# Kernel optimization log

Measured on AMD Instinct MI355X. Metric: run time of the kernel, lower is better.

Reference implementation:

```python
import jax, jax.numpy as jnp
import numpy as np

HEADS = 4
HID = 610
KER = 50  # cov2KerSize
NEG_SLOPE = 0.2


def gat_layer(x, src, dst, w, b, att_src, att_dst, n_nodes):
    # x: [N, Fin], w: [HEADS*HID, Fin], att_*: [1, HEADS, HID], b: [HID]
    h = (x @ w.T).reshape(n_nodes, HEADS, HID)               # [N,H,D]
    a_src = (h * att_src).sum(-1)                            # [N,H]
    a_dst = (h * att_dst).sum(-1)                            # [N,H]
    alpha = jax.nn.leaky_relu(a_src[src] + a_dst[dst], NEG_SLOPE)  # [E,H]
    # softmax over edges grouped by destination node
    m = jax.ops.segment_max(alpha, dst, num_segments=n_nodes)
    e = jnp.exp(alpha - m[dst])
    denom = jax.ops.segment_sum(e, dst, num_segments=n_nodes)
    a = e / (denom[dst] + 1e-16)                             # [E,H]
    msg = h[src] * a[:, :, None]                             # [E,H,D]
    out = jax.ops.segment_sum(msg, dst, num_segments=n_nodes)  # [N,H,D]
    return out.mean(axis=1) + b                              # [N,D] (concat=False)


def setup_inputs() -> dict:
    key = jax.random.key(0)
    ks = jax.random.split(key, 16)
    N, E, FIN, NOUT = 20000, 100000, 128, 86
    x = jax.random.normal(ks[0], (N, FIN), dtype=jnp.float32)
    edge_index = jax.random.randint(ks[1], (2, E), 0, N, dtype=jnp.int64)
    def kaiming(k, shape, fan_in):
        return jax.random.normal(k, shape, dtype=jnp.float32) * np.float32(np.sqrt(2.0 / fan_in))
    w0 = kaiming(ks[2], (HEADS * HID, FIN), FIN)
    b0 = jnp.zeros((HID,), jnp.float32)
    att_src0 = kaiming(ks[3], (1, HEADS, HID), HID)
    att_dst0 = kaiming(ks[4], (1, HEADS, HID), HID)
    w2 = kaiming(ks[5], (HEADS * HID, HID), HID)
    b2 = jnp.zeros((HID,), jnp.float32)
    att_src1 = kaiming(ks[6], (1, HEADS, HID), HID)
    att_dst1 = kaiming(ks[7], (1, HEADS, HID), HID)
    w4 = kaiming(ks[8], (1, 1, 2, KER), 2 * KER)
    b4 = jnp.zeros((1,), jnp.float32)
    w6 = kaiming(ks[9], (1, 1, KER), KER)
    b6 = jnp.zeros((1,), jnp.float32)
    w8 = kaiming(ks[10], (NOUT, 512), 512)
    b8 = jnp.zeros((NOUT,), jnp.float32)
    return dict(x=x, edge_index=edge_index, w0=w0, b0=b0, att_src0=att_src0,
                att_dst0=att_dst0, w2=w2, b2=b2, att_src1=att_src1,
                att_dst1=att_dst1, w4=w4, b4=b4, w6=w6, b6=b6, w8=w8, b8=b8)


def reference(x, edge_index, w0, b0, att_src0, att_dst0, w2, b2, att_src1,
              att_dst1, w4, b4, w6, b6, w8, b8):
    N = x.shape[0]
    src, dst = edge_index[0], edge_index[1]
    x1 = jax.nn.relu(gat_layer(x, src, dst, w0, b0, att_src0, att_dst0, N))
    x2 = jax.nn.relu(gat_layer(x1, src, dst, w2, b2, att_src1, att_dst1, N))
    # edge features: cat(src_feat, dst_feat) viewed as [E,1,2,HID]
    ef = jnp.stack([x2[src], x2[dst]], axis=1)[:, None, :, :]  # [E,1,2,HID]
    y = jax.lax.conv_general_dilated(ef, w4, (1, 1), 'VALID',
                                     dimension_numbers=('NCHW', 'OIHW', 'NCHW'))
    y = jax.nn.relu(y + b4[None, :, None, None])               # [E,1,1,561]
    y = y.reshape(-1, HID - KER + 1, 1).transpose(0, 2, 1)     # [E,1,561]
    y = jax.lax.conv_general_dilated(y, w6, (1,), 'VALID',
                                     dimension_numbers=('NCH', 'OIH', 'NCH'))
    y = jax.nn.relu(y + b6[None, :, None])                     # [E,1,512]
    # adaptive_avg_pool1d to 512 is identity since length is already 512
    y = y.reshape(-1, 512)
    return y @ w8.T + b8                                       # [E, num_outputs]
```

## Files before the change

kernel.cpp:

```cpp
#include <hip/hip_runtime.h>
#include <math.h>

#define HEADS 4
#define HID 610
#define HIDP 640
#define FIN 128
#define KER 50
#define NOUT 86
#define NEG_SLOPE 0.2f
#define LDA 40

typedef short bf8_t __attribute__((ext_vector_type(8)));
typedef float f4_t __attribute__((ext_vector_type(4)));

__device__ __forceinline__ ushort f2bf(float f) {
    unsigned u = __float_as_uint(f);
    unsigned r = (u + 0x7FFFu + ((u >> 16) & 1u)) >> 16;
    return (ushort)r;
}
__device__ __forceinline__ float bf2f(ushort b) { return __uint_as_float(((unsigned)b) << 16); }

__global__ void fill_val(float* __restrict__ p, float v, long n) {
    long i = (long)blockIdx.x * blockDim.x + threadIdx.x;
    if (i < n) p[i] = v;
}

__global__ void copy_int(const int* __restrict__ a, int* __restrict__ b, int n) {
    int i = blockIdx.x * blockDim.x + threadIdx.x;
    if (i < n) b[i] = a[i];
}

__global__ void hist_k(const int* __restrict__ ei, int* __restrict__ hist, int E) {
    int e = blockIdx.x * blockDim.x + threadIdx.x;
    if (e < E) atomicAdd(&hist[ei[E + e]], 1);
}

__global__ __launch_bounds__(1024) void scan_k(const int* __restrict__ hist,
                                               int* __restrict__ base, int Nn) {
    __shared__ int tmp[1024];
    __shared__ int carry;
    if (threadIdx.x == 0) carry = 0;
    __syncthreads();
    for (int c0 = 0; c0 < Nn; c0 += 1024) {
        int i = c0 + threadIdx.x;
        int v = (i < Nn) ? hist[i] : 0;
        tmp[threadIdx.x] = v;
        __syncthreads();
        for (int off = 1; off < 1024; off <<= 1) {
            int t = (threadIdx.x >= off) ? tmp[threadIdx.x - off] : 0;
            __syncthreads();
            tmp[threadIdx.x] += t;
            __syncthreads();
        }
        if (i < Nn) base[i] = carry + tmp[threadIdx.x] - v;
        __syncthreads();
        if (threadIdx.x == 1023) carry += tmp[1023];
        __syncthreads();
    }
    if (threadIdx.x == 0) base[Nn] = carry;
}

__global__ void scatter_k(const int* __restrict__ ei, int* __restrict__ cursor,
                          int* __restrict__ esrc, int E) {
    int e = blockIdx.x * blockDim.x + threadIdx.x;
    if (e >= E) return;
    int d = ei[E + e];
    int pos = atomicAdd(&cursor[d], 1);
    esrc[pos] = ei[e];
}

__global__ void split_pad(const float* __restrict__ in, ushort* __restrict__ hi,
                          ushort* __restrict__ lo, int R, int K, int Kp) {
    long i = (long)blockIdx.x * blockDim.x + threadIdx.x;
    if (i >= (long)R * Kp) return;
    int r = (int)(i / Kp), c = (int)(i % Kp);
    float v = (c < K) ? in[(long)r * K + c] : 0.f;
    ushort h = f2bf(v);
    hi[i] = h;
    lo[i] = f2bf(v - bf2f(h));
}

template <int AMODE, bool BIAS>
__global__ __launch_bounds__(256) void gemm_mfma(const float* __restrict__ A,
                                                 const ushort* __restrict__ Aghi,
                                                 const ushort* __restrict__ Aglo,
                                                 const ushort* __restrict__ Bghi,
                                                 const ushort* __restrict__ Bglo,
                                                 const float* __restrict__ bias,
                                                 float* __restrict__ C,
                                                 int M, int N, int Kp) {
    __shared__ __align__(16) ushort Ah[128 * LDA];
    __shared__ __align__(16) ushort Al[128 * LDA];
    __shared__ __align__(16) ushort Bh[128 * LDA];
    __shared__ __align__(16) ushort Bl[128 * LDA];
    int tid = threadIdx.x;
    int wave = tid >> 6, lane = tid & 63;
    int quad = lane >> 4, l16 = lane & 15;
    int wm = wave & 1, wn = wave >> 1;
    int row0 = blockIdx.y * 128, col0 = blockIdx.x * 128;
    f4_t acc[4][4];
#pragma unroll
    for (int i = 0; i < 4; i++)
#pragma unroll
        for (int j = 0; j < 4; j++) acc[i][j] = (f4_t){0.f, 0.f, 0.f, 0.f};

    for (int k0 = 0; k0 < Kp; k0 += 32) {
        if (AMODE == 0) {
#pragma unroll
            for (int q = 0; q < 4; q++) {
                int p = tid + q * 256;
                int r = p >> 3, c4 = (p & 7) << 2;
                int gr = row0 + r;
                float4 v = make_float4(0.f, 0.f, 0.f, 0.f);
                if (gr < M) v = *(const float4*)(A + (size_t)gr * Kp + k0 + c4);
                ushort4 hv, lv;
                hv.x = f2bf(v.x); lv.x = f2bf(v.x - bf2f(hv.x));
                hv.y = f2bf(v.y); lv.y = f2bf(v.y - bf2f(hv.y));
                hv.z = f2bf(v.z); lv.z = f2bf(v.z - bf2f(hv.z));
                hv.w = f2bf(v.w); lv.w = f2bf(v.w - bf2f(hv.w));
                *(ushort4*)&Ah[r * LDA + c4] = hv;
                *(ushort4*)&Al[r * LDA + c4] = lv;
            }
        } else {
#pragma unroll
            for (int q = 0; q < 2; q++) {
                int p = tid + q * 256;
                int r = p >> 2, sg = (p & 3) << 3;
                int gr = row0 + r;
                uint4 vh = make_uint4(0, 0, 0, 0), vl = make_uint4(0, 0, 0, 0);
                if (gr < M) {
                    vh = *(const uint4*)(Aghi + (size_t)gr * Kp + k0 + sg);
                    vl = *(const uint4*)(Aglo + (size_t)gr * Kp + k0 + sg);
                }
                *(uint4*)&Ah[r * LDA + sg] = vh;
                *(uint4*)&Al[r * LDA + sg] = vl;
            }
        }
#pragma unroll
        for (int q = 0; q < 2; q++) {
            int p = tid + q * 256;
            int r = p >> 2, sg = (p & 3) << 3;
            int gr = col0 + r;
            uint4 vh = make_uint4(0, 0, 0, 0), vl = make_uint4(0, 0, 0, 0);
            if (gr < N) {
                vh = *(const uint4*)(Bghi + (size_t)gr * Kp + k0 + sg);
                vl = *(const uint4*)(Bglo + (size_t)gr * Kp + k0 + sg);
            }
            *(uint4*)&Bh[r * LDA + sg] = vh;
            *(uint4*)&Bl[r * LDA + sg] = vl;
        }
        __syncthreads();
        bf8_t ah[4], al[4], bh[4], bl[4];
#pragma unroll
        for (int t = 0; t < 4; t++) {
            int ar = wm * 64 + t * 16 + l16;
            ah[t] = *(const bf8_t*)&Ah[ar * LDA + quad * 8];
            al[t] = *(const bf8_t*)&Al[ar * LDA + quad * 8];
            int br = wn * 64 + t * 16 + l16;
            bh[t] = *(const bf8_t*)&Bh[br * LDA + quad * 8];
            bl[t] = *(const bf8_t*)&Bl[br * LDA + quad * 8];
        }
#pragma unroll
        for (int i = 0; i < 4; i++)
#pragma unroll
            for (int j = 0; j < 4; j++) {
                acc[i][j] = __builtin_amdgcn_mfma_f32_16x16x32_bf16(ah[i], bh[j], acc[i][j], 0, 0, 0);
                acc[i][j] = __builtin_amdgcn_mfma_f32_16x16x32_bf16(al[i], bh[j], acc[i][j], 0, 0, 0);
                acc[i][j] = __builtin_amdgcn_mfma_f32_16x16x32_bf16(ah[i], bl[j], acc[i][j], 0, 0, 0);
            }
        __syncthreads();
    }
#pragma unroll
    for (int i = 0; i < 4; i++) {
#pragma unroll
        for (int r = 0; r < 4; r++) {
            int grow = row0 + wm * 64 + i * 16 + quad * 4 + r;
            if (grow >= M) continue;
#pragma unroll
            for (int j = 0; j < 4; j++) {
                int gcol = col0 + wn * 64 + j * 16 + l16;
                if (gcol >= N) continue;
                float v = acc[i][j][r];
                if (BIAS) v += bias[gcol];
                C[(size_t)grow * N + gcol] = v;
            }
        }
    }
}

__global__ __launch_bounds__(256) void attn_dots(const float* __restrict__ h,
                                                 const float* __restrict__ att_s,
                                                 const float* __restrict__ att_d,
                                                 float* __restrict__ a_src,
                                                 float* __restrict__ a_dst, int Nn) {
    int n = blockIdx.x;
    int head = threadIdx.x >> 6;
    int lane = threadIdx.x & 63;
    const float2* hr = (const float2*)(h + (long)n * (HEADS * HID) + head * HID);
    const float2* as = (const float2*)(att_s + head * HID);
    const float2* ad = (const float2*)(att_d + head * HID);
    float ss = 0.f, sd = 0.f;
    for (int d = lane; d < HID / 2; d += 64) {
        float2 hv = hr[d], av = as[d], dv = ad[d];
        ss += hv.x * av.x + hv.y * av.y;
        sd += hv.x * dv.x + hv.y * dv.y;
    }
    for (int off = 32; off > 0; off >>= 1) {
        ss += __shfl_down(ss, off);
        sd += __shfl_down(sd, off);
    }
    if (lane == 0) {
        a_src[n * HEADS + head] = ss;
        a_dst[n * HEADS + head] = sd;
    }
}

__global__ __launch_bounds__(256) void node_aggregate(
    const float* __restrict__ h, const float* __restrict__ asrc,
    const float* __restrict__ adst, const int* __restrict__ base,
    const int* __restrict__ esrc, const float* __restrict__ bias,
    float* __restrict__ xout, int Nn) {
    int wave = threadIdx.x >> 6, lane = threadIdx.x & 63;
    int n = blockIdx.x * 4 + wave;
    if (n >= Nn) return;
    int b0 = base[n], deg = base[n + 1] - b0;
    float ad[HEADS];
#pragma unroll
    for (int hh = 0; hh < HEADS; hh++) ad[hh] = adst[n * HEADS + hh];
    float m[HEADS] = {-INFINITY, -INFINITY, -INFINITY, -INFINITY};
    for (int eb = 0; eb < deg; eb += 64) {
        int i = eb + lane;
        if (i < deg) {
            int s = esrc[b0 + i];
#pragma unroll
            for (int hh = 0; hh < HEADS; hh++) {
                float v = asrc[s * HEADS + hh] + ad[hh];
                v = v >= 0.f ? v : NEG_SLOPE * v;
                m[hh] = fmaxf(m[hh], v);
            }
        }
    }
#pragma unroll
    for (int off = 32; off > 0; off >>= 1)
#pragma unroll
        for (int hh = 0; hh < HEADS; hh++) m[hh] = fmaxf(m[hh], __shfl_xor(m[hh], off));
    float sden[HEADS] = {0.f, 0.f, 0.f, 0.f};
    for (int eb = 0; eb < deg; eb += 64) {
        int i = eb + lane;
        if (i < deg) {
            int s = esrc[b0 + i];
#pragma unroll
            for (int hh = 0; hh < HEADS; hh++) {
                float v = asrc[s * HEADS + hh] + ad[hh];
                v = v >= 0.f ? v : NEG_SLOPE * v;
                sden[hh] += expf(v - m[hh]);
            }
        }
    }
#pragma unroll
    for (int off = 32; off > 0; off >>= 1)
#pragma unroll
        for (int hh = 0; hh < HEADS; hh++) sden[hh] += __shfl_xor(sden[hh], off);
    float inv[HEADS];
#pragma unroll
    for (int hh = 0; hh < HEADS; hh++) inv[hh] = 0.25f / (sden[hh] + 1e-16f);
    float acc0[10] = {}, acc1[10] = {}, acc2[10] = {}, acc3[10] = {};
    for (int eb = 0; eb < deg; eb += 64) {
        int i = eb + lane;
        int sreg = 0;
        float coef[HEADS] = {0.f, 0.f, 0.f, 0.f};
        if (i < deg) {
            sreg = esrc[b0 + i];
#pragma unroll
            for (int hh = 0; hh < HEADS; hh++) {
                float v = asrc[sreg * HEADS + hh] + ad[hh];
                v = v >= 0.f ? v : NEG_SLOPE * v;
                coef[hh] = expf(v - m[hh]) * inv[hh];
            }
        }
        int cnt = deg - eb < 64 ? deg - eb : 64;
        for (int j = 0; j < cnt; j++) {
            int s = __shfl(sreg, j);
            float c0 = __shfl(coef[0], j), c1 = __shfl(coef[1], j);
            float c2 = __shfl(coef[2], j), c3 = __shfl(coef[3], j);
            const float* hr = h + (size_t)s * (HEADS * HID);
#pragma unroll
            for (int t = 0; t < 10; t++) {
                int d = lane + t * 64;
                if (d < HID) {
                    acc0[t] = fmaf(c0, hr[d], acc0[t]);
                    acc1[t] = fmaf(c1, hr[HID + d], acc1[t]);
                    acc2[t] = fmaf(c2, hr[2 * HID + d], acc2[t]);
                    acc3[t] = fmaf(c3, hr[3 * HID + d], acc3[t]);
                }
            }
        }
    }
    float* orow = xout + (size_t)n * HIDP;
#pragma unroll
    for (int t = 0; t < 10; t++) {
        int d = lane + t * 64;
        if (d < HID) {
            float v = acc0[t] + acc1[t] + acc2[t] + acc3[t] + bias[d];
            orow[d] = v > 0.f ? v : 0.f;
        }
    }
    for (int d = HID + lane; d < HIDP; d += 64) orow[d] = 0.f;
}

__device__ __forceinline__ int ystag(int j) { return j + (j >> 3); }

__global__ __launch_bounds__(256) void edge_conv(const float* __restrict__ x2,
                                                 const int* __restrict__ ei,
                                                 const float* __restrict__ w4,
                                                 const float* __restrict__ b4,
                                                 const float* __restrict__ w6,
                                                 const float* __restrict__ b6,
                                                 ushort* __restrict__ zhi,
                                                 ushort* __restrict__ zlo, int E) {
    __shared__ __align__(16) float s[4][628];
    __shared__ __align__(16) float t[4][628];
    __shared__ __align__(16) float y[4][652];
    int wave = threadIdx.x >> 6;
    int lane = threadIdx.x & 63;
    int e = blockIdx.x * 4 + wave;
    bool active = (e < E);
    if (active) {
        int sidx = ei[e];
        int didx = ei[E + e];
        const float2* sp = (const float2*)(x2 + (long)sidx * HIDP);
        const float2* tp = (const float2*)(x2 + (long)didx * HIDP);
        float2* sl = (float2*)s[wave];
        float2* tl = (float2*)t[wave];
        for (int i = lane; i < HID / 2; i += 64) {
            sl[i] = sp[i];
            tl[i] = tp[i];
        }
    }
    __syncthreads();
    float bb4 = b4[0], bb6 = b6[0];
    if (active) {
        int j0 = lane * 9;
        float acc[9], sw[9], tw[9];
#pragma unroll
        for (int i = 0; i < 9; i++) {
            acc[i] = bb4;
            sw[i] = s[wave][j0 + i];
            tw[i] = t[wave][j0 + i];
        }
#pragma unroll
        for (int k = 0; k < KER; k++) {
            float ws_ = w4[k], wt_ = w4[KER + k];
#pragma unroll
            for (int i = 0; i < 9; i++) acc[i] += sw[i] * ws_ + tw[i] * wt_;
#pragma unroll
            for (int i = 0; i < 8; i++) {
                sw[i] = sw[i + 1];
                tw[i] = tw[i + 1];
            }
            sw[8] = s[wave][j0 + 9 + k];
            tw[8] = t[wave][j0 + 9 + k];
        }
#pragma unroll
        for (int i = 0; i < 9; i++)
            y[wave][ystag(j0 + i)] = acc[i] > 0.f ? acc[i] : 0.f;
    }
    __syncthreads();
    if (active) {
        int j0 = lane * 8;
        float acc[8], yw[8];
#pragma unroll
        for (int i = 0; i < 8; i++) {
            acc[i] = bb6;
            yw[i] = y[wave][ystag(j0 + i)];
        }
#pragma unroll
        for (int k = 0; k < KER; k++) {
            float wv = w6[k];
#pragma unroll
            for (int i = 0; i < 8; i++) acc[i] += yw[i] * wv;
#pragma unroll
            for (int i = 0; i < 7; i++) yw[i] = yw[i + 1];
            yw[7] = y[wave][ystag(j0 + 8 + k)];
        }
        ushort4 zh0, zh1, zl0, zl1;
        float v;
        v = acc[0] > 0.f ? acc[0] : 0.f; zh0.x = f2bf(v); zl0.x = f2bf(v - bf2f(zh0.x));
        v = acc[1] > 0.f ? acc[1] : 0.f; zh0.y = f2bf(v); zl0.y = f2bf(v - bf2f(zh0.y));
        v = acc[2] > 0.f ? acc[2] : 0.f; zh0.z = f2bf(v); zl0.z = f2bf(v - bf2f(zh0.z));
        v = acc[3] > 0.f ? acc[3] : 0.f; zh0.w = f2bf(v); zl0.w = f2bf(v - bf2f(zh0.w));
        v = acc[4] > 0.f ? acc[4] : 0.f; zh1.x = f2bf(v); zl1.x = f2bf(v - bf2f(zh1.x));
        v = acc[5] > 0.f ? acc[5] : 0.f; zh1.y = f2bf(v); zl1.y = f2bf(v - bf2f(zh1.y));
        v = acc[6] > 0.f ? acc[6] : 0.f; zh1.z = f2bf(v); zl1.z = f2bf(v - bf2f(zh1.z));
        v = acc[7] > 0.f ? acc[7] : 0.f; zh1.w = f2bf(v); zl1.w = f2bf(v - bf2f(zh1.w));
        size_t zo = (size_t)e * 512 + j0;
        *(ushort4*)&zhi[zo] = zh0;
        *(ushort4*)&zhi[zo + 4] = zh1;
        *(ushort4*)&zlo[zo] = zl0;
        *(ushort4*)&zlo[zo + 4] = zl1;
    }
}

extern "C" void kernel_launch(void* const* d_in, const int* in_sizes, int n_in,
                              void* d_out, int out_size, void* d_ws, size_t ws_size,
                              hipStream_t stream) {
    const float* x = (const float*)d_in[0];
    const int* ei = (const int*)d_in[1];
    const float* w0 = (const float*)d_in[2];
    const float* b0 = (const float*)d_in[3];
    const float* att_s0 = (const float*)d_in[4];
    const float* att_d0 = (const float*)d_in[5];
    const float* w2 = (const float*)d_in[6];
    const float* b2 = (const float*)d_in[7];
    const float* att_s1 = (const float*)d_in[8];
    const float* att_d1 = (const float*)d_in[9];
    const float* w4 = (const float*)d_in[10];
    const float* b4 = (const float*)d_in[11];
    const float* w6 = (const float*)d_in[12];
    const float* b6 = (const float*)d_in[13];
    const float* w8 = (const float*)d_in[14];
    const float* b8 = (const float*)d_in[15];
    float* out = (float*)d_out;

    const int Nn = in_sizes[0] / FIN;
    const int E = in_sizes[1] / 2;
    const int HD = HEADS * HID;

    float* ws = (float*)d_ws;
    size_t o = 0;
    float* buf1 = ws + o; o += (size_t)Nn * HIDP;
    ushort* w8hi = (ushort*)(ws + o);
    ushort* w8lo = w8hi + (size_t)NOUT * 512; o += (size_t)NOUT * 512;
    ushort* zhi = (ushort*)(ws + o);
    ushort* zlo = zhi + (size_t)E * 512;
    int* base = (int*)(ws + o); o += (size_t)Nn + 4;
    int* cursor = (int*)(ws + o); o += (size_t)Nn;
    int* esrc = (int*)(ws + o); o += (size_t)E;
    float* asrc = ws + o; o += (size_t)Nn * HEADS;
    float* adst = ws + o; o += (size_t)Nn * HEADS;
    ushort* w0hi = (ushort*)(ws + o);
    ushort* w0lo = w0hi + (size_t)HD * FIN; o += (size_t)HD * FIN;
    ushort* w2hi = (ushort*)(ws + o);
    ushort* w2lo = w2hi + (size_t)HD * HIDP; o += (size_t)HD * HIDP;
    float* h = ws + o;

    int edgeGrid = (E + 255) / 256;
    int nodeWaveGrid = (Nn + 3) / 4;
    int edgeConvGrid = (E + 3) / 4;
    dim3 gGemmL((HD + 127) / 128, (Nn + 127) / 128);
    dim3 gGemmF((NOUT + 127) / 128, (E + 127) / 128);

    split_pad<<<((HD * FIN) + 255) / 256, 256, 0, stream>>>(w0, w0hi, w0lo, HD, FIN, FIN);
    split_pad<<<((HD * HIDP) + 255) / 256, 256, 0, stream>>>(w2, w2hi, w2lo, HD, HID, HIDP);
    split_pad<<<((NOUT * 512) + 255) / 256, 256, 0, stream>>>(w8, w8hi, w8lo, NOUT, 512, 512);
    fill_val<<<(Nn + 255) / 256, 256, 0, stream>>>((float*)cursor, 0.f, Nn);
    hist_k<<<edgeGrid, 256, 0, stream>>>(ei, cursor, E);
    scan_k<<<1, 1024, 0, stream>>>(cursor, base, Nn);
    copy_int<<<(Nn + 255) / 256, 256, 0, stream>>>(base, cursor, Nn);
    scatter_k<<<edgeGrid, 256, 0, stream>>>(ei, cursor, esrc, E);

    gemm_mfma<0, false><<<gGemmL, 256, 0, stream>>>(x, nullptr, nullptr, w0hi, w0lo, nullptr,
                                                    h, Nn, HD, FIN);
    attn_dots<<<Nn, 256, 0, stream>>>(h, att_s0, att_d0, asrc, adst, Nn);
    node_aggregate<<<nodeWaveGrid, 256, 0, stream>>>(h, asrc, adst, base, esrc, b0, buf1, Nn);

    gemm_mfma<0, false><<<gGemmL, 256, 0, stream>>>(buf1, nullptr, nullptr, w2hi, w2lo, nullptr,
                                                    h, Nn, HD, HIDP);
    attn_dots<<<Nn, 256, 0, stream>>>(h, att_s1, att_d1, asrc, adst, Nn);
    node_aggregate<<<nodeWaveGrid, 256, 0, stream>>>(h, asrc, adst, base, esrc, b2, buf1, Nn);

    edge_conv<<<edgeConvGrid, 256, 0, stream>>>(buf1, ei, w4, b4, w6, b6, zhi, zlo, E);

    gemm_mfma<1, true><<<gGemmF, 256, 0, stream>>>(nullptr, zhi, zlo, w8hi, w8lo, b8,
                                                   out, E, NOUT, 512);
}
```

Baseline: 1.308 ms.

## Prefetch GEMM tiles into registers, swizzle LDS, and pre-split layer-1 output to bf16

The MFMA GEMM now loads the next K-tile from global memory into registers while the current tile is computed, so only one barrier pair sits between tiles. The padded LDS stride is replaced by an XOR swizzle to avoid bank conflicts with less shared memory. The first node_aggregate writes bf16 hi/lo halves directly, so the second layer's GEMM reads pre-split bf16 instead of converting fp32 in each block. This adds register pressure for the prefetch buffers and reuses buf1's storage for the hi/lo arrays.

```diff
diff --git a/kernel.cpp b/kernel.cpp
--- a/kernel.cpp
+++ b/kernel.cpp
@@ -8,7 +8,6 @@
 #define KER 50
 #define NOUT 86
 #define NEG_SLOPE 0.2f
-#define LDA 40
 
 typedef short bf8_t __attribute__((ext_vector_type(8)));
 typedef float f4_t __attribute__((ext_vector_type(4)));
@@ -89,76 +88,122 @@
                                                  const float* __restrict__ bias,
                                                  float* __restrict__ C,
                                                  int M, int N, int Kp) {
-    __shared__ __align__(16) ushort Ah[128 * LDA];
-    __shared__ __align__(16) ushort Al[128 * LDA];
-    __shared__ __align__(16) ushort Bh[128 * LDA];
-    __shared__ __align__(16) ushort Bl[128 * LDA];
+    __shared__ __align__(16) ushort Ah[128 * 32];
+    __shared__ __align__(16) ushort Al[128 * 32];
+    __shared__ __align__(16) ushort Bh[128 * 32];
+    __shared__ __align__(16) ushort Bl[128 * 32];
     int tid = threadIdx.x;
     int wave = tid >> 6, lane = tid & 63;
     int quad = lane >> 4, l16 = lane & 15;
     int wm = wave & 1, wn = wave >> 1;
     int row0 = blockIdx.y * 128, col0 = blockIdx.x * 128;
-    f4_t acc[4][4];
-#pragma unroll
-    for (int i = 0; i < 4; i++)
-#pragma unroll
-        for (int j = 0; j < 4; j++) acc[i][j] = (f4_t){0.f, 0.f, 0.f, 0.f};
-
-    for (int k0 = 0; k0 < Kp; k0 += 32) {
+
+    float4 pa0[4];
+    uint4 pah[2], pal[2], pbh[2], pbl[2];
+
+    auto loadA = [&](int k0) {
         if (AMODE == 0) {
 #pragma unroll
             for (int q = 0; q < 4; q++) {
                 int p = tid + q * 256;
                 int r = p >> 3, c4 = (p & 7) << 2;
                 int gr = row0 + r;
-                float4 v = make_float4(0.f, 0.f, 0.f, 0.f);
-                if (gr < M) v = *(const float4*)(A + (size_t)gr * Kp + k0 + c4);
+                pa0[q] = (gr < M) ? *(const float4*)(A + (size_t)gr * Kp + k0 + c4)
+                                  : make_float4(0.f, 0.f, 0.f, 0.f);
+            }
+        } else {
+#pragma unroll
+            for (int q = 0; q < 2; q++) {
+                int p = tid + q * 256;
+                int r = p >> 2, c = p & 3;
+                int gr = row0 + r;
+                if (gr < M) {
+                    pah[q] = *(const uint4*)(Aghi + (size_t)gr * Kp + k0 + c * 8);
+                    pal[q] = *(const uint4*)(Aglo + (size_t)gr * Kp + k0 + c * 8);
+                } else {
+                    pah[q] = make_uint4(0, 0, 0, 0);
+                    pal[q] = make_uint4(0, 0, 0, 0);
+                }
+            }
+        }
+    };
+    auto loadB = [&](int k0) {
+#pragma unroll
+        for (int q = 0; q < 2; q++) {
+            int p = tid + q * 256;
+            int r = p >> 2, c = p & 3;
+            int gr = col0 + r;
+            if (gr < N) {
+                pbh[q] = *(const uint4*)(Bghi + (size_t)gr * Kp + k0 + c * 8);
+                pbl[q] = *(const uint4*)(Bglo + (size_t)gr * Kp + k0 + c * 8);
+            } else {
+                pbh[q] = make_uint4(0, 0, 0, 0);
+                pbl[q] = make_uint4(0, 0, 0, 0);
+            }
+        }
+    };
+    auto writeLDS = [&]() {
+        if (AMODE == 0) {
+#pragma unroll
+            for (int q = 0; q < 4; q++) {
+                int p = tid + q * 256;
+                int r = p >> 3, m = p & 7;
+                int pos = r * 32 + ((((m >> 1)) ^ ((r >> 1) & 3)) << 3) + ((m & 1) << 2);
+                float4 v = pa0[q];
                 ushort4 hv, lv;
                 hv.x = f2bf(v.x); lv.x = f2bf(v.x - bf2f(hv.x));
                 hv.y = f2bf(v.y); lv.y = f2bf(v.y - bf2f(hv.y));
                 hv.z = f2bf(v.z); lv.z = f2bf(v.z - bf2f(hv.z));
                 hv.w = f2bf(v.w); lv.w = f2bf(v.w - bf2f(hv.w));
-                *(ushort4*)&Ah[r * LDA + c4] = hv;
-                *(ushort4*)&Al[r * LDA + c4] = lv;
+                *(ushort4*)&Ah[pos] = hv;
+                *(ushort4*)&Al[pos] = lv;
             }
         } else {
 #pragma unroll
             for (int q = 0; q < 2; q++) {
                 int p = tid + q * 256;
-                int r = p >> 2, sg = (p & 3) << 3;
-                int gr = row0 + r;
-                uint4 vh = make_uint4(0, 0, 0, 0), vl = make_uint4(0, 0, 0, 0);
-                if (gr < M) {
-                    vh = *(const uint4*)(Aghi + (size_t)gr * Kp + k0 + sg);
-                    vl = *(const uint4*)(Aglo + (size_t)gr * Kp + k0 + sg);
-                }
-                *(uint4*)&Ah[r * LDA + sg] = vh;
-                *(uint4*)&Al[r * LDA + sg] = vl;
+                int r = p >> 2, c = p & 3;
+                int pos = r * 32 + ((c ^ ((r >> 1) & 3)) << 3);
+                *(uint4*)&Ah[pos] = pah[q];
+                *(uint4*)&Al[pos] = pal[q];
             }
         }
 #pragma unroll
         for (int q = 0; q < 2; q++) {
             int p = tid + q * 256;
-            int r = p >> 2, sg = (p & 3) << 3;
-            int gr = col0 + r;
-            uint4 vh = make_uint4(0, 0, 0, 0), vl = make_uint4(0, 0, 0, 0);
-            if (gr < N) {
-                vh = *(const uint4*)(Bghi + (size_t)gr * Kp + k0 + sg);
-                vl = *(const uint4*)(Bglo + (size_t)gr * Kp + k0 + sg);
-            }
-            *(uint4*)&Bh[r * LDA + sg] = vh;
-            *(uint4*)&Bl[r * LDA + sg] = vl;
-        }
+            int r = p >> 2, c = p & 3;
+            int pos = r * 32 + ((c ^ ((r >> 1) & 3)) << 3);
+            *(uint4*)&Bh[pos] = pbh[q];
+            *(uint4*)&Bl[pos] = pbl[q];
+        }
+    };
+
+    f4_t acc[4][4];
+#pragma unroll
+    for (int i = 0; i < 4; i++)
+#pragma unroll
+        for (int j = 0; j < 4; j++) acc[i][j] = (f4_t){0.f, 0.f, 0.f, 0.f};
+
+    loadA(0);
+    loadB(0);
+    int sw = (quad ^ ((l16 >> 1) & 3)) << 3;
+    for (int k0 = 0; k0 < Kp; k0 += 32) {
         __syncthreads();
+        writeLDS();
+        __syncthreads();
+        if (k0 + 32 < Kp) {
+            loadA(k0 + 32);
+            loadB(k0 + 32);
+        }
         bf8_t ah[4], al[4], bh[4], bl[4];
 #pragma unroll
         for (int t = 0; t < 4; t++) {
             int ar = wm * 64 + t * 16 + l16;
-            ah[t] = *(const bf8_t*)&Ah[ar * LDA + quad * 8];
-            al[t] = *(const bf8_t*)&Al[ar * LDA + quad * 8];
+            ah[t] = *(const bf8_t*)&Ah[ar * 32 + sw];
+            al[t] = *(const bf8_t*)&Al[ar * 32 + sw];
             int br = wn * 64 + t * 16 + l16;
-            bh[t] = *(const bf8_t*)&Bh[br * LDA + quad * 8];
-            bl[t] = *(const bf8_t*)&Bl[br * LDA + quad * 8];
+            bh[t] = *(const bf8_t*)&Bh[br * 32 + sw];
+            bl[t] = *(const bf8_t*)&Bl[br * 32 + sw];
         }
 #pragma unroll
         for (int i = 0; i < 4; i++)
@@ -168,7 +213,6 @@
                 acc[i][j] = __builtin_amdgcn_mfma_f32_16x16x32_bf16(al[i], bh[j], acc[i][j], 0, 0, 0);
                 acc[i][j] = __builtin_amdgcn_mfma_f32_16x16x32_bf16(ah[i], bl[j], acc[i][j], 0, 0, 0);
             }
-        __syncthreads();
     }
 #pragma unroll
     for (int i = 0; i < 4; i++) {
@@ -215,11 +259,13 @@
     }
 }
 
+template <int OUTMODE>
 __global__ __launch_bounds__(256) void node_aggregate(
     const float* __restrict__ h, const float* __restrict__ asrc,
     const float* __restrict__ adst, const int* __restrict__ base,
     const int* __restrict__ esrc, const float* __restrict__ bias,
-    float* __restrict__ xout, int Nn) {
+    float* __restrict__ xout, ushort* __restrict__ xhi, ushort* __restrict__ xlo,
+    int Nn) {
     int wave = threadIdx.x >> 6, lane = threadIdx.x & 63;
     int n = blockIdx.x * 4 + wave;
     if (n >= Nn) return;
@@ -296,16 +342,29 @@
             }
         }
     }
-    float* orow = xout + (size_t)n * HIDP;
 #pragma unroll
     for (int t = 0; t < 10; t++) {
         int d = lane + t * 64;
         if (d < HID) {
             float v = acc0[t] + acc1[t] + acc2[t] + acc3[t] + bias[d];
-            orow[d] = v > 0.f ? v : 0.f;
-        }
-    }
-    for (int d = HID + lane; d < HIDP; d += 64) orow[d] = 0.f;
+            v = v > 0.f ? v : 0.f;
+            if (OUTMODE == 0) {
+                xout[(size_t)n * HIDP + d] = v;
+            } else {
+                ushort hv = f2bf(v);
+                xhi[(size_t)n * HIDP + d] = hv;
+                xlo[(size_t)n * HIDP + d] = f2bf(v - bf2f(hv));
+            }
+        }
+    }
+    for (int d = HID + lane; d < HIDP; d += 64) {
+        if (OUTMODE == 0) {
+            xout[(size_t)n * HIDP + d] = 0.f;
+        } else {
+            xhi[(size_t)n * HIDP + d] = 0;
+            xlo[(size_t)n * HIDP + d] = 0;
+        }
+    }
 }
 
 __device__ __forceinline__ int ystag(int j) { return j + (j >> 3); }
@@ -429,6 +488,8 @@
     float* ws = (float*)d_ws;
     size_t o = 0;
     float* buf1 = ws + o; o += (size_t)Nn * HIDP;
+    ushort* x1hi = (ushort*)buf1;
+    ushort* x1lo = x1hi + (size_t)Nn * HIDP;
     ushort* w8hi = (ushort*)(ws + o);
     ushort* w8lo = w8hi + (size_t)NOUT * 512; o += (size_t)NOUT * 512;
     ushort* zhi = (ushort*)(ws + o);
@@ -462,12 +523,14 @@
     gemm_mfma<0, false><<<gGemmL, 256, 0, stream>>>(x, nullptr, nullptr, w0hi, w0lo, nullptr,
                                                     h, Nn, HD, FIN);
     attn_dots<<<Nn, 256, 0, stream>>>(h, att_s0, att_d0, asrc, adst, Nn);
-    node_aggregate<<<nodeWaveGrid, 256, 0, stream>>>(h, asrc, adst, base, esrc, b0, buf1, Nn);
-
-    gemm_mfma<0, false><<<gGemmL, 256, 0, stream>>>(buf1, nullptr, nullptr, w2hi, w2lo, nullptr,
+    node_aggregate<1><<<nodeWaveGrid, 256, 0, stream>>>(h, asrc, adst, base, esrc, b0,
+                                                        nullptr, x1hi, x1lo, Nn);
+
+    gemm_mfma<1, false><<<gGemmL, 256, 0, stream>>>(nullptr, x1hi, x1lo, w2hi, w2lo, nullptr,
                                                     h, Nn, HD, HIDP);
     attn_dots<<<Nn, 256, 0, stream>>>(h, att_s1, att_d1, asrc, adst, Nn);
-    node_aggregate<<<nodeWaveGrid, 256, 0, stream>>>(h, asrc, adst, base, esrc, b2, buf1, Nn);
+    node_aggregate<0><<<nodeWaveGrid, 256, 0, stream>>>(h, asrc, adst, base, esrc, b2,
+                                                        buf1, nullptr, nullptr, Nn);
 
     edge_conv<<<edgeConvGrid, 256, 0, stream>>>(buf1, ei, w4, b4, w6, b6, zhi, zlo, E);
 
```

Measured after the change: 1.169 ms. 1.12x faster.
